# Kernel optimization log

Measured on AMD Instinct MI355X. Metric: run time of the kernel, lower is better.

The kernel has to match this reference:

```python
import jax, jax.numpy as jnp
import numpy as np

DIM = 1024
HEADS = 16
DIM_HEAD = 64
SCALE = DIM_HEAD ** -0.5


def setup_inputs() -> dict:
    key = jax.random.key(0)
    k1, k2, k3, k4 = jax.random.split(key, 4)
    B, N = 2, 2048
    x = jax.random.normal(k1, (B, N, DIM), dtype=jnp.float32)
    mask = jnp.ones((B, N), dtype=bool)
    gamma = jnp.ones((DIM,), dtype=jnp.float32)
    # init like nn.Linear default ~ U(-1/sqrt(fan_in), 1/sqrt(fan_in)); gaussian * 0.02 is fine numerically
    Wq = jax.random.normal(k2, (DIM, HEADS * DIM_HEAD), dtype=jnp.float32) * 0.02
    Wkv = jax.random.normal(k3, (DIM, HEADS * DIM_HEAD * 2), dtype=jnp.float32) * 0.02
    Wo = jax.random.normal(k4, (HEADS * DIM_HEAD, DIM), dtype=jnp.float32) * 0.02
    return {"x": x, "mask": mask, "gamma": gamma, "Wq": Wq, "Wkv": Wkv, "Wo": Wo}


def _rmsnorm(x, gamma):
    # F.normalize(x, dim=-1) * sqrt(dim) * gamma ; eps clamp matches torch (1e-12)
    n = jnp.sqrt(jnp.sum(x * x, axis=-1, keepdims=True))
    return x / jnp.maximum(n, 1e-12) * (DIM ** 0.5) * gamma


def reference(x, mask, gamma, Wq, Wkv, Wo):
    B, N, _ = x.shape
    xn = _rmsnorm(x, gamma)
    q = xn @ Wq                      # [b, n, h*d]
    kv = xn @ Wkv                    # [b, n, 2*h*d] (self-attention: context = x)
    k, v = jnp.split(kv, 2, axis=-1)

    def to_heads(t):
        return t.reshape(B, N, HEADS, DIM_HEAD).transpose(0, 2, 1, 3)  # b h n d

    q, k, v = to_heads(q), to_heads(k), to_heads(v)

    sim = jnp.einsum('bhid,bhjd->bhij', q, k) * SCALE
    neg = -jnp.finfo(sim.dtype).max
    # key padding mask: b j -> b 1 1 j
    sim = jnp.where(mask[:, None, None, :], sim, neg)
    # causal: triu(j - i + 1) with i == j -> strict upper triangle masked
    causal_mask = jnp.triu(jnp.ones((N, N), dtype=bool), k=1)
    sim = jnp.where(causal_mask, neg, sim)

    attn = jax.nn.softmax(sim, axis=-1)
    out = jnp.einsum('bhij,bhjd->bhid', attn, v)
    out = out.transpose(0, 2, 1, 3).reshape(B, N, HEADS * DIM_HEAD)
    return out @ Wo
```

## Files before the change

kernel.cpp:

```cpp
#include <hip/hip_runtime.h>
#include <hip/hip_bf16.h>
#include <stdint.h>

#define NSEQ 2048
#define NB 2
#define NTOK (NB*NSEQ)

typedef __attribute__((ext_vector_type(8))) short bf16x8;
typedef __attribute__((ext_vector_type(4))) float f32x4;

#if __has_builtin(__builtin_amdgcn_exp2f)
#define EXP2F(x) __builtin_amdgcn_exp2f(x)
#else
#define EXP2F(x) __expf((x) * 0.69314718056f)
#endif

__device__ __forceinline__ unsigned short f2bf(float f) {
  __hip_bfloat16 h = __float2bfloat16(f);
  return *reinterpret_cast<unsigned short*>(&h);
}

__device__ __forceinline__ unsigned cvt_pk_bf16(float a, float b) {
  unsigned r;
  asm("v_cvt_pk_bf16_f32 %0, %1, %2" : "=v"(r) : "v"(a), "v"(b));
  return r;
}

__device__ __forceinline__ void gload_lds16(const void* g, void* l) {
  __builtin_amdgcn_global_load_lds(
      (const __attribute__((address_space(1))) void*)(uintptr_t)g,
      (__attribute__((address_space(3))) void*)(uintptr_t)l,
      16, 0, 0);
}

__global__ __launch_bounds__(256) void rmsnorm_cast(
    const float* __restrict__ x, const float* __restrict__ gamma,
    unsigned short* __restrict__ xn)
{
  const int row = blockIdx.x;
  const float4 v = ((const float4*)(x + (size_t)row*1024))[threadIdx.x];
  float ss = v.x*v.x + v.y*v.y + v.z*v.z + v.w*v.w;
  #pragma unroll
  for (int o = 32; o >= 1; o >>= 1) ss += __shfl_xor(ss, o);
  __shared__ float wsum[4];
  if ((threadIdx.x & 63) == 0) wsum[threadIdx.x >> 6] = ss;
  __syncthreads();
  const float tot = wsum[0] + wsum[1] + wsum[2] + wsum[3];
  const float f = 32.0f / fmaxf(sqrtf(tot), 1e-12f);
  const float4 g = ((const float4*)gamma)[threadIdx.x];
  ushort4 o;
  o.x = f2bf(v.x * f * g.x);
  o.y = f2bf(v.y * f * g.y);
  o.z = f2bf(v.z * f * g.z);
  o.w = f2bf(v.w * f * g.w);
  ((ushort4*)(xn + (size_t)row*1024))[threadIdx.x] = o;
}

__global__ __launch_bounds__(256) void transpose_cast_all(
    const float* __restrict__ Wq, const float* __restrict__ Wkv,
    const float* __restrict__ Wo, unsigned short* __restrict__ WallT,
    unsigned short* __restrict__ WoT, float qscale)
{
  const int bx = blockIdx.x;
  const float* src; unsigned short* dst; int C; float scale; int cblk;
  if (bx < 16)      { src = Wq;  dst = WallT;               C = 1024; scale = qscale; cblk = bx; }
  else if (bx < 48) { src = Wkv; dst = WallT + 1024*1024;   C = 2048; scale = 1.0f;   cblk = bx - 16; }
  else              { src = Wo;  dst = WoT;                 C = 1024; scale = 1.0f;   cblk = bx - 48; }

  __shared__ float t[64][65];
  const int lx = threadIdx.x & 63, ly = threadIdx.x >> 6;
  const int c0 = cblk * 64, r0 = blockIdx.y * 64;
  #pragma unroll
  for (int i = 0; i < 16; ++i) {
    const int r = ly + i*4;
    t[r][lx] = src[(size_t)(r0 + r)*C + c0 + lx];
  }
  __syncthreads();
  #pragma unroll
  for (int i = 0; i < 16; ++i) {
    const int r = ly + i*4;
    dst[(size_t)(c0 + r)*1024 + r0 + lx] = f2bf(t[lx][r] * scale);
  }
}

template<int MODE>
__global__ __launch_bounds__(512, 2) void gemm_bt256(
    const unsigned short* __restrict__ A, const unsigned short* __restrict__ BT,
    void* __restrict__ Cp, unsigned short* __restrict__ Vt, int M, int N, int K)
{
  __shared__ __align__(16) unsigned short As[3][256*32];
  __shared__ __align__(16) unsigned short Bs[3][256*32];
  const int tid = threadIdx.x, lane = tid & 63, wv = tid >> 6;
  const int wm = wv >> 2, wn = wv & 3;
  const int m0 = blockIdx.y * 256, n0 = blockIdx.x * 256;
  const int g = lane >> 4, l15 = lane & 15;

  f32x4 acc[8][4];
  #pragma unroll
  for (int i = 0; i < 8; ++i)
    #pragma unroll
    for (int j = 0; j < 4; ++j) acc[i][j] = f32x4{0.f,0.f,0.f,0.f};

  auto STAGE = [&](int buf, int kt) {
    const int k0 = kt * 32;
    #pragma unroll
    for (int j = 0; j < 2; ++j) {
      const int c = wv*128 + j*64 + lane;
      const int row = c >> 2;
      const int kc = (c & 3) ^ ((row >> 1) & 3);
      gload_lds16(A  + (size_t)(m0 + row)*K + k0 + kc*8, As[buf] + (size_t)(wv*128 + j*64)*8);
      gload_lds16(BT + (size_t)(n0 + row)*K + k0 + kc*8, Bs[buf] + (size_t)(wv*128 + j*64)*8);
    }
  };

  const int nk = K >> 5;
  STAGE(0, 0);
  STAGE(1, 1);
  int cur = 0, sb = 2;
  for (int kt = 0; kt < nk; ++kt) {
    if (kt + 1 < nk) { asm volatile("s_waitcnt vmcnt(4)" ::: "memory"); }
    else             { asm volatile("s_waitcnt vmcnt(0)" ::: "memory"); }
    __builtin_amdgcn_s_barrier();
    __builtin_amdgcn_sched_barrier(0);

    bf16x8 af[8], bfr[4];
    #pragma unroll
    for (int mt = 0; mt < 8; ++mt) {
      const int row = wm*128 + mt*16 + l15;
      af[mt] = *(const bf16x8*)(As[cur] + row*32 + ((g ^ ((row >> 1) & 3)) << 3));
    }
    #pragma unroll
    for (int nt = 0; nt < 4; ++nt) {
      const int col = wn*64 + nt*16 + l15;
      bfr[nt] = *(const bf16x8*)(Bs[cur] + col*32 + ((g ^ ((col >> 1) & 3)) << 3));
    }
    if (kt + 2 < nk) STAGE(sb, kt + 2);
    #pragma unroll
    for (int mt = 0; mt < 8; ++mt)
      #pragma unroll
      for (int nt = 0; nt < 4; ++nt)
        acc[mt][nt] = __builtin_amdgcn_mfma_f32_16x16x32_bf16(af[mt], bfr[nt], acc[mt][nt], 0, 0, 0);

    cur = (cur == 2) ? 0 : cur + 1;
    sb  = (sb  == 2) ? 0 : sb  + 1;
  }

  if (MODE == 2 && n0 >= 2048) {
    #pragma unroll
    for (int mt = 0; mt < 8; ++mt)
      #pragma unroll
      for (int nt = 0; nt < 4; ++nt) {
        const int row = m0 + wm*128 + mt*16 + g*4;
        const int col = n0 + wn*64 + nt*16 + l15;
        const f32x4 v = acc[mt][nt];
        ushort4 o;
        o.x = f2bf(v[0]); o.y = f2bf(v[1]); o.z = f2bf(v[2]); o.w = f2bf(v[3]);
        *(ushort4*)(Vt + ((size_t)((row >> 11)*1024 + (col - 2048)))*2048 + (row & 2047)) = o;
      }
    return;
  }

  #pragma unroll
  for (int mt = 0; mt < 8; ++mt)
    #pragma unroll
    for (int nt = 0; nt < 4; ++nt) {
      const int row = m0 + wm*128 + mt*16 + g*4;
      const int col = n0 + wn*64 + nt*16 + l15;
      const f32x4 v = acc[mt][nt];
      #pragma unroll
      for (int r = 0; r < 4; ++r)
        ((unsigned short*)Cp)[(size_t)(row + r)*N + col] = f2bf(v[r]);
    }
}

template<int MODE>
__global__ __launch_bounds__(256) void gemm_bt(
    const unsigned short* __restrict__ A, const unsigned short* __restrict__ BT,
    void* __restrict__ Cp, unsigned short* __restrict__ Vt, int M, int N, int K)
{
  __shared__ __align__(16) unsigned short As[3][128*32];
  __shared__ __align__(16) unsigned short Bs[3][128*32];
  const int tid = threadIdx.x, lane = tid & 63, wv = tid >> 6;
  const int wm = wv >> 1, wn = wv & 1;

  const int nbx = gridDim.x;
  int bid = blockIdx.y * nbx + blockIdx.x;
  const int cpx = (nbx * gridDim.y) >> 3;
  bid = (bid & 7) * cpx + (bid >> 3);
  const int m0 = (bid / nbx) * 128, n0 = (bid % nbx) * 128;

  const int g = lane >> 4, l15 = lane & 15;

  f32x4 acc[4][4];
  #pragma unroll
  for (int i = 0; i < 4; ++i)
    #pragma unroll
    for (int j = 0; j < 4; ++j) acc[i][j] = f32x4{0.f,0.f,0.f,0.f};

  auto STAGE = [&](int buf, int kt) {
    const int k0 = kt * 32;
    #pragma unroll
    for (int j = 0; j < 2; ++j) {
      const int c = wv*128 + j*64 + lane;
      const int row = c >> 2;
      const int kc = (c & 3) ^ ((row >> 1) & 3);
      gload_lds16(A  + (size_t)(m0 + row)*K + k0 + kc*8, As[buf] + (size_t)(wv*128 + j*64)*8);
      gload_lds16(BT + (size_t)(n0 + row)*K + k0 + kc*8, Bs[buf] + (size_t)(wv*128 + j*64)*8);
    }
  };

  const int nk = K >> 5;
  STAGE(0, 0);
  STAGE(1, 1);
  int cur = 0, sb = 2;
  for (int kt = 0; kt < nk; ++kt) {
    if (kt + 1 < nk) { asm volatile("s_waitcnt vmcnt(4)" ::: "memory"); }
    else             { asm volatile("s_waitcnt vmcnt(0)" ::: "memory"); }
    __builtin_amdgcn_s_barrier();
    __builtin_amdgcn_sched_barrier(0);

    bf16x8 af[4], bfr[4];
    #pragma unroll
    for (int mt = 0; mt < 4; ++mt) {
      const int row = wm*64 + mt*16 + l15;
      af[mt] = *(const bf16x8*)(As[cur] + row*32 + ((g ^ ((row >> 1) & 3)) << 3));
    }
    #pragma unroll
    for (int nt = 0; nt < 4; ++nt) {
      const int col = wn*64 + nt*16 + l15;
      bfr[nt] = *(const bf16x8*)(Bs[cur] + col*32 + ((g ^ ((col >> 1) & 3)) << 3));
    }
    if (kt + 2 < nk) STAGE(sb, kt + 2);
    #pragma unroll
    for (int mt = 0; mt < 4; ++mt)
      #pragma unroll
      for (int nt = 0; nt < 4; ++nt)
        acc[mt][nt] = __builtin_amdgcn_mfma_f32_16x16x32_bf16(af[mt], bfr[nt], acc[mt][nt], 0, 0, 0);

    cur = (cur == 2) ? 0 : cur + 1;
    sb  = (sb  == 2) ? 0 : sb  + 1;
  }

  #pragma unroll
  for (int mt = 0; mt < 4; ++mt)
    #pragma unroll
    for (int nt = 0; nt < 4; ++nt) {
      const int row = m0 + wm*64 + mt*16 + g*4;
      const int col = n0 + wn*64 + nt*16 + l15;
      const f32x4 v = acc[mt][nt];
      #pragma unroll
      for (int r = 0; r < 4; ++r) {
        if (MODE != 0) ((unsigned short*)Cp)[(size_t)(row + r)*N + col] = f2bf(v[r]);
        else           ((float*)Cp)[(size_t)(row + r)*N + col] = v[r];
      }
    }
}

__global__ __launch_bounds__(512, 4) void attn_fwd(
    const unsigned short* __restrict__ QKV,
    const unsigned short* __restrict__ Vt,
    unsigned short* __restrict__ AO)
{
  __shared__ __align__(16) unsigned char smem[81920];

  const int bh = blockIdx.x, k = blockIdx.y;
  const int qlo = k, qhi = 31 - k;
  const int b = bh >> 4, h = bh & 15;
  const int tid = threadIdx.x, lane = tid & 63, wv = tid >> 6;
  const int quad = wv >> 2, w4 = wv & 3;
  const int g = lane >> 4, q15 = lane & 15;
  const int qrow_lo = qlo*64 + w4*16 + q15;
  const int qrow_hi = qhi*64 + w4*16 + q15;

  unsigned short* Kb = (unsigned short*)(smem + quad*32768);
  unsigned short* Vb = (unsigned short*)(smem + quad*32768 + 16384);
  unsigned short* Plw = (unsigned short*)(smem + 65536 + wv*2048);

  const unsigned short* Qlo = QKV + (size_t)(b*NSEQ + qrow_lo)*3072 + h*64;
  const unsigned short* Qhi = QKV + (size_t)(b*NSEQ + qrow_hi)*3072 + h*64;
  const bf16x8 qlo0 = *(const bf16x8*)(Qlo + g*8);
  const bf16x8 qlo1 = *(const bf16x8*)(Qlo + 32 + g*8);
  const bf16x8 qhi0 = *(const bf16x8*)(Qhi + g*8);
  const bf16x8 qhi1 = *(const bf16x8*)(Qhi + 32 + g*8);

  const bf16x8 ones = { (short)0x3F80, (short)0x3F80, (short)0x3F80, (short)0x3F80,
                        (short)0x3F80, (short)0x3F80, (short)0x3F80, (short)0x3F80 };

  f32x4 l_lo = f32x4{0.f,0.f,0.f,0.f}, l_hi = f32x4{0.f,0.f,0.f,0.f};
  f32x4 olo[4], ohi[4];
  #pragma unroll
  for (int i = 0; i < 4; ++i) { olo[i] = f32x4{0.f,0.f,0.f,0.f}; ohi[i] = f32x4{0.f,0.f,0.f,0.f}; }

  auto STAGE = [&](int buf, int kt) {
    const int kv0 = kt * 64;
    #pragma unroll
    for (int j = 0; j < 2; ++j) {
      const int c = w4*128 + j*64 + lane;
      const int row = c >> 3;
      const int kc = (c & 7) ^ (row & 7);
      gload_lds16(QKV + (size_t)(b*NSEQ + kv0 + row)*3072 + 1024 + h*64 + kc*8,
                  Kb + (size_t)buf*4096 + (size_t)(w4*128 + j*64)*8);
      gload_lds16(Vt + (size_t)(bh*64 + row)*NSEQ + kv0 + kc*8,
                  Vb + (size_t)buf*4096 + (size_t)(w4*128 + j*64)*8);
    }
  };

  auto COMPUTE = [&](const bf16x8& qf0, const bf16x8& qf1, int qrow,
                     f32x4& lacc, f32x4* oacc, bool diag, int cur, int kv0) {
    f32x4 s[4];
    const unsigned short* Kc = Kb + (size_t)cur*4096;
    __builtin_amdgcn_s_setprio(1);
    #pragma unroll
    for (int st = 0; st < 4; ++st) {
      f32x4 a = f32x4{0.f,0.f,0.f,0.f};
      const int row = st*16 + q15;
      const int sw = row & 7;
      const bf16x8 kf0 = *(const bf16x8*)(Kc + row*64 + ((g ^ sw) << 3));
      const bf16x8 kf1 = *(const bf16x8*)(Kc + row*64 + (((4 | g) ^ sw) << 3));
      a = __builtin_amdgcn_mfma_f32_16x16x32_bf16(kf0, qf0, a, 0, 0, 0);
      a = __builtin_amdgcn_mfma_f32_16x16x32_bf16(kf1, qf1, a, 0, 0, 0);
      s[st] = a;
    }
    __builtin_amdgcn_s_setprio(0);

    if (diag) {
      #pragma unroll
      for (int st = 0; st < 4; ++st)
        #pragma unroll
        for (int r = 0; r < 4; ++r) {
          const int kvg = kv0 + st*16 + g*4 + r;
          if (kvg > qrow) s[st][r] = -1e30f;
        }
    }

    #pragma unroll
    for (int st = 0; st < 4; ++st) {
      const float p0 = EXP2F(s[st][0] - 12.0f);
      const float p1 = EXP2F(s[st][1] - 12.0f);
      const float p2 = EXP2F(s[st][2] - 12.0f);
      const float p3 = EXP2F(s[st][3] - 12.0f);
      const int base = (q15 << 6) + ((((st << 1) | (g >> 1)) ^ (q15 & 7)) << 3) + ((g & 1) << 2);
      uint2 w;
      w.x = cvt_pk_bf16(p0, p1);
      w.y = cvt_pk_bf16(p2, p3);
      *(uint2*)(Plw + base) = w;
    }

    const unsigned short* Vc = Vb + (size_t)cur*4096;
    __builtin_amdgcn_s_setprio(1);
    #pragma unroll
    for (int ks = 0; ks < 2; ++ks) {
      const bf16x8 pf = *(const bf16x8*)(Plw + (q15 << 6) + ((((ks << 2) | g) ^ (q15 & 7)) << 3));
      lacc = __builtin_amdgcn_mfma_f32_16x16x32_bf16(pf, ones, lacc, 0, 0, 0);
      #pragma unroll
      for (int dt = 0; dt < 4; ++dt) {
        const int dr = dt*16 + q15;
        const bf16x8 vf = *(const bf16x8*)(Vc + dr*64 + ((((ks << 2) | g) ^ (dr & 7)) << 3));
        oacc[dt] = __builtin_amdgcn_mfma_f32_16x16x32_bf16(pf, vf, oacc[dt], 0, 0, 0);
      }
    }
    __builtin_amdgcn_s_setprio(0);
  };

  STAGE(0, quad);
  __syncthreads();
  int cur = 0;
  for (int i = 0; i < 16; ++i) {
    const int t = quad + 2*i;
    const int tn = t + 2;
    if (tn <= qhi) STAGE(cur ^ 1, tn);
    if (t <= qhi) COMPUTE(qhi0, qhi1, qrow_hi, l_hi, ohi, t == qhi, cur, t*64);
    if (t <= qlo) COMPUTE(qlo0, qlo1, qrow_lo, l_lo, olo, t == qlo, cur, t*64);
    __syncthreads();
    cur ^= 1;
  }

  float* OHI = (float*)smem;
  float* OLO = (float*)(smem + 16384);
  float* LH  = (float*)(smem + 32768);
  float* LL  = (float*)(smem + 33024);

  if (quad == 1) {
    #pragma unroll
    for (int dt = 0; dt < 4; ++dt) {
      *(f32x4*)(OHI + ((w4*64 + lane)*4 + dt)*4) = ohi[dt];
      *(f32x4*)(OLO + ((w4*64 + lane)*4 + dt)*4) = olo[dt];
    }
    if (q15 == 0) {
      #pragma unroll
      for (int r = 0; r < 4; ++r) {
        LH[w4*16 + g*4 + r] = l_hi[r];
        LL[w4*16 + g*4 + r] = l_lo[r];
      }
    }
  }
  __syncthreads();
  if (quad == 0) {
    f32x4 ph[4], pl[4];
    #pragma unroll
    for (int dt = 0; dt < 4; ++dt) {
      ph[dt] = *(const f32x4*)(OHI + ((w4*64 + lane)*4 + dt)*4);
      pl[dt] = *(const f32x4*)(OLO + ((w4*64 + lane)*4 + dt)*4);
    }
    #pragma unroll
    for (int r = 0; r < 4; ++r) {
      const int row = g*4 + r;
      {
        const float inv = 1.0f / (l_hi[r] + LH[w4*16 + row]);
        const int qr = qhi*64 + w4*16 + row;
        #pragma unroll
        for (int dt = 0; dt < 4; ++dt)
          AO[(size_t)(b*NSEQ + qr)*1024 + h*64 + dt*16 + q15] =
              f2bf((ohi[dt][r] + ph[dt][r]) * inv);
      }
      {
        const float inv = 1.0f / (l_lo[r] + LL[w4*16 + row]);
        const int qr = qlo*64 + w4*16 + row;
        #pragma unroll
        for (int dt = 0; dt < 4; ++dt)
          AO[(size_t)(b*NSEQ + qr)*1024 + h*64 + dt*16 + q15] =
              f2bf((olo[dt][r] + pl[dt][r]) * inv);
      }
    }
  }
}

extern "C" void kernel_launch(void* const* d_in, const int* in_sizes, int n_in,
                              void* d_out, int out_size, void* d_ws, size_t ws_size,
                              hipStream_t stream) {
  (void)in_sizes; (void)n_in; (void)out_size; (void)ws_size;
  const float* x     = (const float*)d_in[0];
  const float* gamma = (const float*)d_in[2];
  const float* Wq    = (const float*)d_in[3];
  const float* Wkv   = (const float*)d_in[4];
  const float* Wo    = (const float*)d_in[5];
  float* out = (float*)d_out;

  char* ws = (char*)d_ws;
  unsigned short* xn    = (unsigned short*)(ws);
  unsigned short* AO    = xn;
  unsigned short* WallT = (unsigned short*)(ws + (size_t)(8u  << 20));
  unsigned short* WoT   = (unsigned short*)(ws + (size_t)(14u << 20));
  unsigned short* QKV   = (unsigned short*)(ws + (size_t)(16u << 20));
  unsigned short* Vt    = (unsigned short*)(ws + (size_t)(40u << 20));

  const float QSCALE = 0.125f * 1.44269504f;

  rmsnorm_cast<<<NTOK, 256, 0, stream>>>(x, gamma, xn);
  transpose_cast_all<<<dim3(64, 16), 256, 0, stream>>>(Wq, Wkv, Wo, WallT, WoT, QSCALE);
  gemm_bt256<2><<<dim3(3072/256, 4096/256), 512, 0, stream>>>(xn, WallT, (void*)QKV, Vt, 4096, 3072, 1024);
  attn_fwd<<<dim3(32, 16), 512, 0, stream>>>(QKV, Vt, AO);
  gemm_bt<0><<<dim3(1024/128, 4096/128), 256, 0, stream>>>(AO, WoT, (void*)out, nullptr, 4096, 1024, 1024);
}
```

Before: 94.27 us.

## Fuse rmsnorm and weight cast kernels; retile QKV GEMM to 128x128 two-wave blocks

Merges the rmsnorm/cast and weight transpose/cast kernels into one launch, with blocks dispatched by block index, to save a kernel launch. Replaces the 256x256, 8-wave QKV GEMM with 128x128 tiles computed by 2 waves of 128 threads, each wave holding a 128x64 accumulator. This gives 768 blocks instead of 192 for better CU fill, at the cost of less data reuse per block and fewer waves to hide latency. The staging loop and the vmcnt wait are adjusted for the extra loads per thread.

```diff
diff --git a/kernel.cpp b/kernel.cpp
--- a/kernel.cpp
+++ b/kernel.cpp
@@ -33,43 +33,42 @@
       16, 0, 0);
 }
 
-__global__ __launch_bounds__(256) void rmsnorm_cast(
+__global__ __launch_bounds__(256) void prep_fused(
     const float* __restrict__ x, const float* __restrict__ gamma,
-    unsigned short* __restrict__ xn)
-{
-  const int row = blockIdx.x;
-  const float4 v = ((const float4*)(x + (size_t)row*1024))[threadIdx.x];
-  float ss = v.x*v.x + v.y*v.y + v.z*v.z + v.w*v.w;
-  #pragma unroll
-  for (int o = 32; o >= 1; o >>= 1) ss += __shfl_xor(ss, o);
-  __shared__ float wsum[4];
-  if ((threadIdx.x & 63) == 0) wsum[threadIdx.x >> 6] = ss;
-  __syncthreads();
-  const float tot = wsum[0] + wsum[1] + wsum[2] + wsum[3];
-  const float f = 32.0f / fmaxf(sqrtf(tot), 1e-12f);
-  const float4 g = ((const float4*)gamma)[threadIdx.x];
-  ushort4 o;
-  o.x = f2bf(v.x * f * g.x);
-  o.y = f2bf(v.y * f * g.y);
-  o.z = f2bf(v.z * f * g.z);
-  o.w = f2bf(v.w * f * g.w);
-  ((ushort4*)(xn + (size_t)row*1024))[threadIdx.x] = o;
-}
-
-__global__ __launch_bounds__(256) void transpose_cast_all(
+    unsigned short* __restrict__ xn,
     const float* __restrict__ Wq, const float* __restrict__ Wkv,
     const float* __restrict__ Wo, unsigned short* __restrict__ WallT,
     unsigned short* __restrict__ WoT, float qscale)
 {
-  const int bx = blockIdx.x;
+  __shared__ float t[64][65];
+  const int bid = blockIdx.x;
+  if (bid < NTOK) {
+    const int row = bid;
+    const float4 v = ((const float4*)(x + (size_t)row*1024))[threadIdx.x];
+    float ss = v.x*v.x + v.y*v.y + v.z*v.z + v.w*v.w;
+    #pragma unroll
+    for (int o = 32; o >= 1; o >>= 1) ss += __shfl_xor(ss, o);
+    if ((threadIdx.x & 63) == 0) t[0][threadIdx.x >> 6] = ss;
+    __syncthreads();
+    const float tot = t[0][0] + t[0][1] + t[0][2] + t[0][3];
+    const float f = 32.0f / fmaxf(sqrtf(tot), 1e-12f);
+    const float4 g = ((const float4*)gamma)[threadIdx.x];
+    ushort4 o;
+    o.x = f2bf(v.x * f * g.x);
+    o.y = f2bf(v.y * f * g.y);
+    o.z = f2bf(v.z * f * g.z);
+    o.w = f2bf(v.w * f * g.w);
+    ((ushort4*)(xn + (size_t)row*1024))[threadIdx.x] = o;
+    return;
+  }
+  const int tb = bid - NTOK;
+  const int bx = tb & 63, by = tb >> 6;
   const float* src; unsigned short* dst; int C; float scale; int cblk;
   if (bx < 16)      { src = Wq;  dst = WallT;               C = 1024; scale = qscale; cblk = bx; }
   else if (bx < 48) { src = Wkv; dst = WallT + 1024*1024;   C = 2048; scale = 1.0f;   cblk = bx - 16; }
   else              { src = Wo;  dst = WoT;                 C = 1024; scale = 1.0f;   cblk = bx - 48; }
-
-  __shared__ float t[64][65];
   const int lx = threadIdx.x & 63, ly = threadIdx.x >> 6;
-  const int c0 = cblk * 64, r0 = blockIdx.y * 64;
+  const int c0 = cblk * 64, r0 = by * 64;
   #pragma unroll
   for (int i = 0; i < 16; ++i) {
     const int r = ly + i*4;
@@ -84,15 +83,14 @@
 }
 
 template<int MODE>
-__global__ __launch_bounds__(512, 2) void gemm_bt256(
+__global__ __launch_bounds__(128, 1) void gemm_w2(
     const unsigned short* __restrict__ A, const unsigned short* __restrict__ BT,
     void* __restrict__ Cp, unsigned short* __restrict__ Vt, int M, int N, int K)
 {
-  __shared__ __align__(16) unsigned short As[3][256*32];
-  __shared__ __align__(16) unsigned short Bs[3][256*32];
+  __shared__ __align__(16) unsigned short As[3][128*32];
+  __shared__ __align__(16) unsigned short Bs[3][128*32];
   const int tid = threadIdx.x, lane = tid & 63, wv = tid >> 6;
-  const int wm = wv >> 2, wn = wv & 3;
-  const int m0 = blockIdx.y * 256, n0 = blockIdx.x * 256;
+  const int m0 = blockIdx.y * 128, n0 = blockIdx.x * 128;
   const int g = lane >> 4, l15 = lane & 15;
 
   f32x4 acc[8][4];
@@ -104,12 +102,12 @@
   auto STAGE = [&](int buf, int kt) {
     const int k0 = kt * 32;
     #pragma unroll
-    for (int j = 0; j < 2; ++j) {
-      const int c = wv*128 + j*64 + lane;
+    for (int j = 0; j < 4; ++j) {
+      const int c = j*128 + wv*64 + lane;
       const int row = c >> 2;
       const int kc = (c & 3) ^ ((row >> 1) & 3);
-      gload_lds16(A  + (size_t)(m0 + row)*K + k0 + kc*8, As[buf] + (size_t)(wv*128 + j*64)*8);
-      gload_lds16(BT + (size_t)(n0 + row)*K + k0 + kc*8, Bs[buf] + (size_t)(wv*128 + j*64)*8);
+      gload_lds16(A  + (size_t)(m0 + row)*K + k0 + kc*8, As[buf] + (size_t)(j*128 + wv*64)*8);
+      gload_lds16(BT + (size_t)(n0 + row)*K + k0 + kc*8, Bs[buf] + (size_t)(j*128 + wv*64)*8);
     }
   };
 
@@ -118,7 +116,7 @@
   STAGE(1, 1);
   int cur = 0, sb = 2;
   for (int kt = 0; kt < nk; ++kt) {
-    if (kt + 1 < nk) { asm volatile("s_waitcnt vmcnt(4)" ::: "memory"); }
+    if (kt + 1 < nk) { asm volatile("s_waitcnt vmcnt(8)" ::: "memory"); }
     else             { asm volatile("s_waitcnt vmcnt(0)" ::: "memory"); }
     __builtin_amdgcn_s_barrier();
     __builtin_amdgcn_sched_barrier(0);
@@ -126,12 +124,12 @@
     bf16x8 af[8], bfr[4];
     #pragma unroll
     for (int mt = 0; mt < 8; ++mt) {
-      const int row = wm*128 + mt*16 + l15;
+      const int row = mt*16 + l15;
       af[mt] = *(const bf16x8*)(As[cur] + row*32 + ((g ^ ((row >> 1) & 3)) << 3));
     }
     #pragma unroll
     for (int nt = 0; nt < 4; ++nt) {
-      const int col = wn*64 + nt*16 + l15;
+      const int col = wv*64 + nt*16 + l15;
       bfr[nt] = *(const bf16x8*)(Bs[cur] + col*32 + ((g ^ ((col >> 1) & 3)) << 3));
     }
     if (kt + 2 < nk) STAGE(sb, kt + 2);
@@ -150,8 +148,8 @@
     for (int mt = 0; mt < 8; ++mt)
       #pragma unroll
       for (int nt = 0; nt < 4; ++nt) {
-        const int row = m0 + wm*128 + mt*16 + g*4;
-        const int col = n0 + wn*64 + nt*16 + l15;
+        const int row = m0 + mt*16 + g*4;
+        const int col = n0 + wv*64 + nt*16 + l15;
         const f32x4 v = acc[mt][nt];
         ushort4 o;
         o.x = f2bf(v[0]); o.y = f2bf(v[1]); o.z = f2bf(v[2]); o.w = f2bf(v[3]);
@@ -164,8 +162,8 @@
   for (int mt = 0; mt < 8; ++mt)
     #pragma unroll
     for (int nt = 0; nt < 4; ++nt) {
-      const int row = m0 + wm*128 + mt*16 + g*4;
-      const int col = n0 + wn*64 + nt*16 + l15;
+      const int row = m0 + mt*16 + g*4;
+      const int col = n0 + wv*64 + nt*16 + l15;
       const f32x4 v = acc[mt][nt];
       #pragma unroll
       for (int r = 0; r < 4; ++r)
@@ -446,9 +444,8 @@
 
   const float QSCALE = 0.125f * 1.44269504f;
 
-  rmsnorm_cast<<<NTOK, 256, 0, stream>>>(x, gamma, xn);
-  transpose_cast_all<<<dim3(64, 16), 256, 0, stream>>>(Wq, Wkv, Wo, WallT, WoT, QSCALE);
-  gemm_bt256<2><<<dim3(3072/256, 4096/256), 512, 0, stream>>>(xn, WallT, (void*)QKV, Vt, 4096, 3072, 1024);
+  prep_fused<<<NTOK + 1024, 256, 0, stream>>>(x, gamma, xn, Wq, Wkv, Wo, WallT, WoT, QSCALE);
+  gemm_w2<2><<<dim3(3072/128, 4096/128), 128, 0, stream>>>(xn, WallT, (void*)QKV, Vt, 4096, 3072, 1024);
   attn_fwd<<<dim3(32, 16), 512, 0, stream>>>(QKV, Vt, AO);
   gemm_bt<0><<<dim3(1024/128, 4096/128), 256, 0, stream>>>(AO, WoT, (void*)out, nullptr, 4096, 1024, 1024);
 }
```

New measurement: 98.52 us. +4.5%, slower.
